# Optimization experiments

Hardware: AMD Instinct MI355X
Metric: run time of the kernel (lower is better)

The kernel has to match this reference:

```python
import jax, jax.numpy as jnp
import numpy as np

B, S, D, H = 2, 2048, 1024, 16
HD = D // H
SCALE = HD ** -0.5


def _xavier(key, fan_out, fan_in):
    limit = (6.0 / (fan_in + fan_out)) ** 0.5
    return jax.random.uniform(key, (fan_out, fan_in), jnp.float32, -limit, limit)


def setup_inputs() -> dict:
    key = jax.random.key(0)
    ks = jax.random.split(key, 11)
    return {
        "q": jax.random.normal(ks[0], (B, S, D), jnp.float32),
        "k": jax.random.normal(ks[1], (B, S, D), jnp.float32),
        "v": jax.random.normal(ks[2], (B, S, D), jnp.float32),
        "Wq": _xavier(ks[3], D, D), "bq": jnp.zeros((D,), jnp.float32),
        "Wk": _xavier(ks[4], D, D), "bk": jnp.zeros((D,), jnp.float32),
        "Wv": _xavier(ks[5], D, D), "bv": jnp.zeros((D,), jnp.float32),
        "Wo": _xavier(ks[6], D, D), "bo": jnp.zeros((D,), jnp.float32),
    }


def reference(q, k, v, Wq, bq, Wk, bk, Wv, bv, Wo, bo):
    # projections: torch Linear is x @ W.T + b
    def split_heads(x):  # [B,S,D] -> [B,H,S,HD]
        return x.reshape(B, S, H, HD).transpose(0, 2, 1, 3)

    qh = split_heads(q @ Wq.T + bq)
    kh = split_heads(k @ Wk.T + bk)
    vh = split_heads(v @ Wv.T + bv)

    scores = jnp.einsum('bhqd,bhkd->bhqk', qh, kh) * SCALE  # [B,H,S,S]
    attn = jax.nn.softmax(scores, axis=-1)
    out = jnp.einsum('bhqk,bhkd->bhqd', attn, vh)  # [B,H,S,HD]
    out = out.transpose(0, 2, 1, 3).reshape(B, S, D)
    return out @ Wo.T + bo
```

## Files before the change

kernel.cpp:

```cpp
#include <hip/hip_runtime.h>
#include <hip/hip_bf16.h>

typedef __attribute__((ext_vector_type(8))) short bf16x8;
typedef __attribute__((ext_vector_type(4))) float f32x4;
typedef __attribute__((ext_vector_type(16))) float f32x16;
typedef unsigned short u16;

#define MFMA16(A,B,C) __builtin_amdgcn_mfma_f32_16x16x32_bf16(A,B,C,0,0,0)
#define MFMA32(A,B,C) __builtin_amdgcn_mfma_f32_32x32x16_bf16(A,B,C,0,0,0)

__device__ __forceinline__ u16 f2bf(float f) {
    union { float f; unsigned u; } x{f};
    unsigned r = x.u + 0x7FFFu + ((x.u >> 16) & 1u);
    return (u16)(r >> 16);
}

__device__ __forceinline__ unsigned cvtpk(float lo, float hi) {
    unsigned r;
    asm("v_cvt_pk_bf16_f32 %0, %1, %2" : "=v"(r) : "v"(lo), "v"(hi));
    return r;
}

__device__ __forceinline__ void gload16(const void* src, void* dst) {
    __builtin_amdgcn_global_load_lds((const __attribute__((address_space(1))) void*)src,
                                     (__attribute__((address_space(3))) void*)dst, 16, 0, 0);
}

__device__ __forceinline__ void xhalf(unsigned lo, unsigned hi2, int hf, unsigned& j0, unsigned& j2) {
#if __has_builtin(__builtin_amdgcn_permlane32_swap)
    auto r = __builtin_amdgcn_permlane32_swap(lo, hi2, false, false);
    j0 = r[0]; j2 = r[1];
#else
    unsigned olo = (unsigned)__shfl_xor((int)lo, 32);
    unsigned ohi = (unsigned)__shfl_xor((int)hi2, 32);
    j0 = hf ? ohi : lo;
    j2 = hf ? hi2 : olo;
#endif
}

__global__ __launch_bounds__(256)
void cvt_all(const float* __restrict__ q, const float* __restrict__ k, const float* __restrict__ v,
             const float* __restrict__ Wq, const float* __restrict__ Wk,
             const float* __restrict__ Wv, const float* __restrict__ Wo,
             u16* __restrict__ oq, u16* __restrict__ ok, u16* __restrict__ ov,
             u16* __restrict__ ow) {
    int blk = blockIdx.x;
    const float* s;
    u16* o;
    if (blk < 6144) {
        int which = blk >> 11, lb = blk & 2047;
        s = (which == 0 ? q : (which == 1 ? k : v)) + (size_t)lb * 2048;
        o = (which == 0 ? oq : (which == 1 ? ok : ov)) + (size_t)lb * 2048;
    } else {
        int wblk = blk - 6144;
        int which = wblk >> 9, lb = wblk & 511;
        s = (which == 0 ? Wq : (which == 1 ? Wk : (which == 2 ? Wv : Wo))) + (size_t)lb * 2048;
        o = ow + (size_t)which * 1048576 + (size_t)lb * 2048;
    }
    size_t base = (size_t)threadIdx.x * 8;
    float4 v0 = *(const float4*)(s + base);
    float4 v1 = *(const float4*)(s + base + 4);
    bf16x8 rv;
    rv[0] = (short)f2bf(v0.x); rv[1] = (short)f2bf(v0.y); rv[2] = (short)f2bf(v0.z); rv[3] = (short)f2bf(v0.w);
    rv[4] = (short)f2bf(v1.x); rv[5] = (short)f2bf(v1.y); rv[6] = (short)f2bf(v1.z); rv[7] = (short)f2bf(v1.w);
    *(bf16x8*)(o + base) = rv;
}

template<int MODE>
__device__ __forceinline__ void gemm_body(u16* gsm, const u16* __restrict__ A, const u16* __restrict__ W,
                                          const float* __restrict__ bias, void* __restrict__ Cout,
                                          float scale) {
    u16* Asl = gsm;
    u16* Wsl = gsm + 16384;
    const int t = threadIdx.x;
    const int lane = t & 63, w = t >> 6;
    const int g = lane >> 4, c = lane & 15;
    const int bm = blockIdx.y * 128, bn = blockIdx.x * 64;
    const int wr = (w >> 1) * 64, wc = (w & 1) * 32;

    f32x4 acc[4][2];
    #pragma unroll
    for (int i = 0; i < 4; ++i) {
        acc[i][0] = f32x4{0.f, 0.f, 0.f, 0.f};
        acc[i][1] = f32x4{0.f, 0.f, 0.f, 0.f};
    }

#define GS(buf, k0)                                                                         \
    {                                                                                       \
        _Pragma("unroll")                                                                   \
        for (int i = 0; i < 4; ++i) {                                                       \
            int off = i * 4096 + w * 1024 + lane * 16;                                      \
            int row = off >> 7, sl = (off >> 4) & 7;                                        \
            gload16(A + (size_t)(bm + row) * 1024 + (k0) + ((sl ^ (row & 7)) << 3),         \
                    Asl + (buf) * 8192 + i * 2048 + w * 512);                               \
        }                                                                                   \
        _Pragma("unroll")                                                                   \
        for (int i = 0; i < 2; ++i) {                                                       \
            int off = i * 4096 + w * 1024 + lane * 16;                                      \
            int row = off >> 7, sl = (off >> 4) & 7;                                        \
            gload16(W + (size_t)(bn + row) * 1024 + (k0) + ((sl ^ (row & 7)) << 3),         \
                    Wsl + (buf) * 4096 + i * 2048 + w * 512);                               \
        }                                                                                   \
    }

    GS(0, 0);
    __syncthreads();
    int cur = 0;

    for (int k0 = 0; k0 < 1024; k0 += 64) {
        if (k0 < 960) GS(cur ^ 1, k0 + 64);
        #pragma unroll
        for (int ks = 0; ks < 2; ++ks) {
            bf16x8 af[4], bfr[2];
            #pragma unroll
            for (int rf = 0; rf < 4; ++rf) {
                int row = wr + rf * 16 + c;
                int col = (ks * 64 + g * 16) ^ ((row & 7) << 4);
                af[rf] = *(const bf16x8*)((const char*)Asl + cur * 16384 + row * 128 + col);
            }
            #pragma unroll
            for (int cf = 0; cf < 2; ++cf) {
                int row = wc + cf * 16 + c;
                int col = (ks * 64 + g * 16) ^ ((row & 7) << 4);
                bfr[cf] = *(const bf16x8*)((const char*)Wsl + cur * 8192 + row * 128 + col);
            }
            __builtin_amdgcn_s_setprio(1);
            #pragma unroll
            for (int rf = 0; rf < 4; ++rf)
                #pragma unroll
                for (int cf = 0; cf < 2; ++cf)
                    acc[rf][cf] = MFMA16(af[rf], bfr[cf], acc[rf][cf]);
            __builtin_amdgcn_s_setprio(0);
        }
        __syncthreads();
        cur ^= 1;
    }
#undef GS

    if (MODE == 2) {
        u16* trp = gsm;
        #pragma unroll
        for (int rf = 0; rf < 4; ++rf)
            #pragma unroll
            for (int cf = 0; cf < 2; ++cf) {
                int d = wc + cf * 16 + c;
                float bv = bias[bn + d];
                unsigned p0 = cvtpk(acc[rf][cf][0] + bv, acc[rf][cf][1] + bv);
                unsigned p1 = cvtpk(acc[rf][cf][2] + bv, acc[rf][cf][3] + bv);
                *(uint2*)&trp[d * 136 + wr + rf * 16 + 4 * g] = make_uint2(p0, p1);
            }
        __syncthreads();
        const int hb = bn >> 6, bb = bm >> 11, sb = bm & 2047;
        u16* vt = (u16*)Cout;
        #pragma unroll
        for (int i = 0; i < 4; ++i) {
            int fl = t + 256 * i;
            int d = fl >> 4, ch = fl & 15;
            bf16x8 vv = *(const bf16x8*)&trp[d * 136 + ch * 8];
            *(bf16x8*)(vt + ((size_t)((bb * 16 + hb) * 64 + d)) * 2048 + sb + ch * 8) = vv;
        }
        return;
    }

    #pragma unroll
    for (int rf = 0; rf < 4; ++rf) {
        #pragma unroll
        for (int cf = 0; cf < 2; ++cf) {
            int nCol = bn + wc + cf * 16 + c;
            float bv = bias[nCol];
            #pragma unroll
            for (int r = 0; r < 4; ++r) {
                int row = bm + wr + rf * 16 + 4 * g + r;
                float val = (acc[rf][cf][r] + bv) * scale;
                if (MODE == 1) ((float*)Cout)[(size_t)row * 1024 + nCol] = val;
                else           ((u16*)Cout)[(size_t)row * 1024 + nCol] = f2bf(val);
            }
        }
    }
}

__global__ __launch_bounds__(256)
void gemm_qkv(const u16* __restrict__ Ab, const u16* __restrict__ Wb,
              const float* __restrict__ b0, const float* __restrict__ b1, const float* __restrict__ b2,
              u16* __restrict__ Qp, u16* __restrict__ Kp, u16* __restrict__ Vtb, float qscale) {
    __shared__ u16 gsm[24576];
    int z = blockIdx.z;
    if (z == 0)      gemm_body<0>(gsm, Ab,           Wb,           b0, Qp,  qscale);
    else if (z == 1) gemm_body<0>(gsm, Ab + 4194304, Wb + 1048576, b1, Kp,  1.f);
    else             gemm_body<2>(gsm, Ab + 8388608, Wb + 2097152, b2, Vtb, 1.f);
}

__global__ __launch_bounds__(256)
void gemm_o(const u16* __restrict__ A, const u16* __restrict__ W,
            const float* __restrict__ bias, float* __restrict__ out) {
    __shared__ u16 gsm[24576];
    gemm_body<1>(gsm, A, W, bias, out, 1.f);
}

__global__ __launch_bounds__(512, 4)
void attn_mfma(const u16* __restrict__ Qp, const u16* __restrict__ Kp,
               const u16* __restrict__ Vt, u16* __restrict__ AO) {
    __shared__ u16 smem[40960];

    const int t = threadIdx.x, lane = t & 63, w = t >> 6;
    const int wl = w & 3, half = w >> 2;
    const int c5 = lane & 31, hf = lane >> 5;

    const int id = blockIdx.x;
    const int xcd = id & 7, slot = id >> 3;
    const int hd = xcd * 4 + (slot >> 4);
    const int b = hd >> 4, h = hd & 15;
    const int qw = (slot & 15) * 128 + wl * 32;

    bf16x8 qfr[4];
    #pragma unroll
    for (int ks = 0; ks < 4; ++ks)
        qfr[ks] = *(const bf16x8*)(Qp + (size_t)(b * 2048 + qw + c5) * 1024 + h * 64 + ks * 16 + hf * 8);

    f32x16 oacc[2], lacc;
    #pragma unroll
    for (int j = 0; j < 16; ++j) { oacc[0][j] = 0.f; oacc[1][j] = 0.f; lacc[j] = 0.f; }

    bf16x8 ones;
    #pragma unroll
    for (int j = 0; j < 8; ++j) ones[j] = (short)0x3F80;

#define STAGE(kbuf, vbuf, it)                                                                       \
    {                                                                                               \
        int row = t >> 3, sl = t & 7;                                                               \
        _Pragma("unroll")                                                                           \
        for (int i = 0; i < 2; ++i) {                                                               \
            int kti = i * 16 + (it);                                                                \
            const u16* srck = Kp + (size_t)(b * 2048 + kti * 64 + row) * 1024 + h * 64 +            \
                              ((sl ^ (row & 7)) << 3);                                              \
            gload16(srck, smem + i * 8192 + (kbuf) * 4096 + w * 512);                               \
            const u16* srcv = Vt + ((size_t)((b * 16 + h) * 64 + row)) * 2048 + kti * 64 +          \
                              ((sl ^ (row & 7)) << 3);                                              \
            gload16(srcv, smem + 16384 + i * 12288 + (vbuf) * 4096 + w * 512);                      \
        }                                                                                           \
    }

#define QKT(kbase, kf, s)                                                                           \
    {                                                                                               \
        _Pragma("unroll")                                                                           \
        for (int j = 0; j < 16; ++j) (s)[j] = 0.f;                                                  \
        const int krow = (kf) * 32 + c5;                                                            \
        const int ksw = (krow & 7) << 4;                                                            \
        _Pragma("unroll")                                                                           \
        for (int ks = 0; ks < 4; ++ks) {                                                            \
            bf16x8 ka = *(const bf16x8*)((kbase) + krow * 128 + ((ks * 32 + hf * 16) ^ ksw));       \
            (s) = MFMA32(ka, qfr[ks], (s));                                                         \
        }                                                                                           \
    }

#define SM(s, pv0, pv1)                                                                             \
    {                                                                                               \
        _Pragma("unroll")                                                                           \
        for (int j = 0; j < 16; ++j) (s)[j] = exp2f((s)[j]);                                        \
        unsigned wd[8];                                                                             \
        _Pragma("unroll")                                                                           \
        for (int j = 0; j < 8; ++j) wd[j] = cvtpk((s)[2 * j], (s)[2 * j + 1]);                      \
        union { unsigned u[4]; bf16x8 v; } a0, a1;                                                  \
        xhalf(wd[0], wd[2], hf, a0.u[0], a0.u[2]);                                                  \
        xhalf(wd[1], wd[3], hf, a0.u[1], a0.u[3]);                                                  \
        xhalf(wd[4], wd[6], hf, a1.u[0], a1.u[2]);                                                  \
        xhalf(wd[5], wd[7], hf, a1.u[1], a1.u[3]);                                                  \
        (pv0) = a0.v; (pv1) = a1.v;                                                                 \
    }

#define PVOP(vbase, kf, pv0, pv1)                                                                   \
    {                                                                                               \
        _Pragma("unroll")                                                                           \
        for (int pp = 0; pp < 2; ++pp) {                                                            \
            bf16x8 pB = pp ? (pv1) : (pv0);                                                         \
            const int kc = (kf) * 64 + pp * 32 + hf * 16;                                           \
            _Pragma("unroll")                                                                       \
            for (int df = 0; df < 2; ++df) {                                                        \
                int vrow = df * 32 + c5;                                                            \
                bf16x8 va = *(const bf16x8*)((vbase) + vrow * 128 + (kc ^ ((vrow & 7) << 4)));      \
                oacc[df] = MFMA32(va, pB, oacc[df]);                                                \
            }                                                                                       \
            lacc = MFMA32(ones, pB, lacc);                                                          \
        }                                                                                           \
    }

    STAGE(0, 0, 0);
    __syncthreads();

    const char* smb = (const char*)smem;
    const char* vreg = smb + 32768 + half * 24576;
    int cur2 = 0, cur3 = 0, nxt3 = 1, prv3 = 2;
    bf16x8 pc0, pc1;

    for (int it = 0; it < 16; ++it) {
        if (it < 15) STAGE(cur2 ^ 1, nxt3, it + 1);
        const char* kbase = smb + half * 16384 + cur2 * 8192;
        const char* vcur = vreg + cur3 * 8192;
        const char* vprev = vreg + prv3 * 8192;

        f32x16 s0;
        __builtin_amdgcn_s_setprio(1);
        QKT(kbase, 0, s0);
        if (it) PVOP(vprev, 1, pc0, pc1);
        __builtin_amdgcn_s_setprio(0);

        bf16x8 b00, b01;
        SM(s0, b00, b01);

        f32x16 s1;
        __builtin_amdgcn_s_setprio(1);
        QKT(kbase, 1, s1);
        PVOP(vcur, 0, b00, b01);
        __builtin_amdgcn_s_setprio(0);

        SM(s1, pc0, pc1);

        __syncthreads();
        prv3 = cur3; cur3 = nxt3; nxt3 = (nxt3 == 2) ? 0 : nxt3 + 1;
        cur2 ^= 1;
    }
    {
        const char* vprev = vreg + prv3 * 8192;
        PVOP(vprev, 1, pc0, pc1);
    }

    __syncthreads();
    float* fs = (float*)smem;
    const int pbase = wl * 2112;
    if (half) {
        #pragma unroll
        for (int df = 0; df < 2; ++df)
            #pragma unroll
            for (int j = 0; j < 16; ++j)
                fs[pbase + (df * 16 + j) * 64 + lane] = oacc[df][j];
        fs[pbase + 2048 + lane] = lacc[0];
    }
    __syncthreads();
    if (!half) {
        #pragma unroll
        for (int df = 0; df < 2; ++df)
            #pragma unroll
            for (int j = 0; j < 16; ++j)
                oacc[df][j] += fs[pbase + (df * 16 + j) * 64 + lane];
        const float inv = 1.f / (lacc[0] + fs[pbase + 2048 + lane]);

        char* pw = (char*)smem + 33792 + wl * 4096;
        #pragma unroll
        for (int df = 0; df < 2; ++df)
            #pragma unroll
            for (int rq = 0; rq < 4; ++rq) {
                unsigned p0 = cvtpk(oacc[df][rq * 4 + 0] * inv, oacc[df][rq * 4 + 1] * inv);
                unsigned p1 = cvtpk(oacc[df][rq * 4 + 2] * inv, oacc[df][rq * 4 + 3] * inv);
                int dbyte = df * 64 + rq * 16 + hf * 8;
                *(uint2*)(pw + c5 * 128 + (dbyte ^ ((c5 & 7) << 4))) = make_uint2(p0, p1);
            }
        #pragma unroll
        for (int i = 0; i < 4; ++i) {
            int fl = lane + 64 * i;
            int q = fl >> 3, ch = fl & 7;
            bf16x8 vv = *(const bf16x8*)(pw + q * 128 + ((ch * 16) ^ ((q & 7) << 4)));
            *(bf16x8*)(AO + (size_t)(b * 2048 + qw + q) * 1024 + h * 64 + ch * 8) = vv;
        }
    }
}

extern "C" void kernel_launch(void* const* d_in, const int* in_sizes, int n_in,
                              void* d_out, int out_size, void* d_ws, size_t ws_size,
                              hipStream_t stream) {
    const float* q  = (const float*)d_in[0];
    const float* k  = (const float*)d_in[1];
    const float* v  = (const float*)d_in[2];
    const float* Wq = (const float*)d_in[3];
    const float* bq = (const float*)d_in[4];
    const float* Wk = (const float*)d_in[5];
    const float* bk = (const float*)d_in[6];
    const float* Wv = (const float*)d_in[7];
    const float* bv = (const float*)d_in[8];
    const float* Wo = (const float*)d_in[9];
    const float* bo = (const float*)d_in[10];

    const size_t NE = 4194304;
    u16* ws = (u16*)d_ws;
    u16* xq = ws;
    u16* xk = ws + NE;
    u16* xv = ws + 2 * NE;
    u16* Wb = ws + 3 * NE;
    u16* Qp = ws + 4 * NE;
    u16* Kp = ws + 5 * NE;
    u16* Vtb = ws + 6 * NE;
    u16* AO = xk;

    const float CS = 0.125f * 1.4426950408889634f;

    cvt_all<<<8192, 256, 0, stream>>>(q, k, v, Wq, Wk, Wv, Wo, xq, xk, xv, Wb);

    gemm_qkv<<<dim3(16, 32, 3), 256, 0, stream>>>(ws, Wb, bq, bk, bv, Qp, Kp, Vtb, CS);

    attn_mfma<<<512, 512, 0, stream>>>(Qp, Kp, Vtb, AO);

    gemm_o<<<dim3(16, 32), 256, 0, stream>>>(AO, Wb + 3145728, bo, (float*)d_out);
}
```

Baseline: 120.9 us.

## Split attention KV halves into separate blocks with combine kernel; XCD-aware GEMM tiling

The attention kernel drops the in-block split across two 4-wave halves. Each KV half now runs as an independent 256-thread block, doubling the grid to 1024 blocks with half the LDS. Each block writes bf16-normalized partial outputs and row sums to workspace, and a new combine kernel merges them weighted by the row sums and writes AO. The GEMM launches are flattened to 1D grids with XCD-aware tile mapping for L2 locality. The price is an extra kernel launch, extra global traffic for the partials, and an added bf16 rounding step on the partial outputs.

```diff
diff --git a/kernel.cpp b/kernel.cpp
--- a/kernel.cpp
+++ b/kernel.cpp
@@ -13,6 +13,12 @@
     union { float f; unsigned u; } x{f};
     unsigned r = x.u + 0x7FFFu + ((x.u >> 16) & 1u);
     return (u16)(r >> 16);
+}
+
+__device__ __forceinline__ float bf2f(u16 x) {
+    union { unsigned u; float f; } y;
+    y.u = ((unsigned)x) << 16;
+    return y.f;
 }
 
 __device__ __forceinline__ unsigned cvtpk(float lo, float hi) {
@@ -69,13 +75,12 @@
 template<int MODE>
 __device__ __forceinline__ void gemm_body(u16* gsm, const u16* __restrict__ A, const u16* __restrict__ W,
                                           const float* __restrict__ bias, void* __restrict__ Cout,
-                                          float scale) {
+                                          float scale, int bm, int bn) {
     u16* Asl = gsm;
     u16* Wsl = gsm + 16384;
     const int t = threadIdx.x;
     const int lane = t & 63, w = t >> 6;
     const int g = lane >> 4, c = lane & 15;
-    const int bm = blockIdx.y * 128, bn = blockIdx.x * 64;
     const int wr = (w >> 1) * 64, wc = (w & 1) * 32;
 
     f32x4 acc[4][2];
@@ -184,33 +189,43 @@
               const float* __restrict__ b0, const float* __restrict__ b1, const float* __restrict__ b2,
               u16* __restrict__ Qp, u16* __restrict__ Kp, u16* __restrict__ Vtb, float qscale) {
     __shared__ u16 gsm[24576];
-    int z = blockIdx.z;
-    if (z == 0)      gemm_body<0>(gsm, Ab,           Wb,           b0, Qp,  qscale);
-    else if (z == 1) gemm_body<0>(gsm, Ab + 4194304, Wb + 1048576, b1, Kp,  1.f);
-    else             gemm_body<2>(gsm, Ab + 8388608, Wb + 2097152, b2, Vtb, 1.f);
+    int id = blockIdx.x;
+    int xcd = id & 7, r = id >> 3;
+    int z = r >> 6, rr = r & 63;
+    int bm = (xcd * 4 + (rr >> 4)) * 128;
+    int bn = (rr & 15) * 64;
+    if (z == 0)      gemm_body<0>(gsm, Ab,           Wb,           b0, Qp,  qscale, bm, bn);
+    else if (z == 1) gemm_body<0>(gsm, Ab + 4194304, Wb + 1048576, b1, Kp,  1.f, bm, bn);
+    else             gemm_body<2>(gsm, Ab + 8388608, Wb + 2097152, b2, Vtb, 1.f, bm, bn);
 }
 
 __global__ __launch_bounds__(256)
 void gemm_o(const u16* __restrict__ A, const u16* __restrict__ W,
             const float* __restrict__ bias, float* __restrict__ out) {
     __shared__ u16 gsm[24576];
-    gemm_body<1>(gsm, A, W, bias, out, 1.f);
-}
-
-__global__ __launch_bounds__(512, 4)
+    int id = blockIdx.x;
+    int xcd = id & 7, r = id >> 3;
+    int bm = (xcd * 4 + (r >> 4)) * 128;
+    int bn = (r & 15) * 64;
+    gemm_body<1>(gsm, A, W, bias, out, 1.f, bm, bn);
+}
+
+__global__ __launch_bounds__(256, 4)
 void attn_mfma(const u16* __restrict__ Qp, const u16* __restrict__ Kp,
-               const u16* __restrict__ Vt, u16* __restrict__ AO) {
-    __shared__ u16 smem[40960];
+               const u16* __restrict__ Vt, u16* __restrict__ op0, u16* __restrict__ op1,
+               float* __restrict__ lpart) {
+    __shared__ u16 smem[20480];
 
     const int t = threadIdx.x, lane = t & 63, w = t >> 6;
-    const int wl = w & 3, half = w >> 2;
     const int c5 = lane & 31, hf = lane >> 5;
 
     const int id = blockIdx.x;
-    const int xcd = id & 7, slot = id >> 3;
-    const int hd = xcd * 4 + (slot >> 4);
+    const int xcd = id & 7, r = id >> 3;
+    const int hd = xcd * 4 + (r >> 5);
+    const int rem = r & 31;
+    const int qblk = rem >> 1, half = rem & 1;
     const int b = hd >> 4, h = hd & 15;
-    const int qw = (slot & 15) * 128 + wl * 32;
+    const int qw = qblk * 128 + w * 32;
 
     bf16x8 qfr[4];
     #pragma unroll
@@ -227,16 +242,17 @@
 
 #define STAGE(kbuf, vbuf, it)                                                                       \
     {                                                                                               \
-        int row = t >> 3, sl = t & 7;                                                               \
-        _Pragma("unroll")                                                                           \
-        for (int i = 0; i < 2; ++i) {                                                               \
-            int kti = i * 16 + (it);                                                                \
+        const int kti = half * 16 + (it);                                                           \
+        _Pragma("unroll")                                                                           \
+        for (int i2 = 0; i2 < 2; ++i2) {                                                            \
+            int cch = t + 256 * i2;                                                                 \
+            int row = cch >> 3, sl = cch & 7;                                                       \
             const u16* srck = Kp + (size_t)(b * 2048 + kti * 64 + row) * 1024 + h * 64 +            \
                               ((sl ^ (row & 7)) << 3);                                              \
-            gload16(srck, smem + i * 8192 + (kbuf) * 4096 + w * 512);                               \
+            gload16(srck, smem + (kbuf) * 4096 + i2 * 2048 + w * 512);                              \
             const u16* srcv = Vt + ((size_t)((b * 16 + h) * 64 + row)) * 2048 + kti * 64 +          \
                               ((sl ^ (row & 7)) << 3);                                              \
-            gload16(srcv, smem + 16384 + i * 12288 + (vbuf) * 4096 + w * 512);                      \
+            gload16(srcv, smem + 8192 + (vbuf) * 4096 + i2 * 2048 + w * 512);                       \
         }                                                                                           \
     }
 
@@ -288,13 +304,13 @@
     __syncthreads();
 
     const char* smb = (const char*)smem;
-    const char* vreg = smb + 32768 + half * 24576;
+    const char* vreg = smb + 16384;
     int cur2 = 0, cur3 = 0, nxt3 = 1, prv3 = 2;
     bf16x8 pc0, pc1;
 
     for (int it = 0; it < 16; ++it) {
         if (it < 15) STAGE(cur2 ^ 1, nxt3, it + 1);
-        const char* kbase = smb + half * 16384 + cur2 * 8192;
+        const char* kbase = smb + cur2 * 8192;
         const char* vcur = vreg + cur3 * 8192;
         const char* vprev = vreg + prv3 * 8192;
 
@@ -324,43 +340,69 @@
         PVOP(vprev, 1, pc0, pc1);
     }
 
-    __syncthreads();
-    float* fs = (float*)smem;
-    const int pbase = wl * 2112;
-    if (half) {
-        #pragma unroll
-        for (int df = 0; df < 2; ++df)
-            #pragma unroll
-            for (int j = 0; j < 16; ++j)
-                fs[pbase + (df * 16 + j) * 64 + lane] = oacc[df][j];
-        fs[pbase + 2048 + lane] = lacc[0];
-    }
-    __syncthreads();
-    if (!half) {
-        #pragma unroll
-        for (int df = 0; df < 2; ++df)
-            #pragma unroll
-            for (int j = 0; j < 16; ++j)
-                oacc[df][j] += fs[pbase + (df * 16 + j) * 64 + lane];
-        const float inv = 1.f / (lacc[0] + fs[pbase + 2048 + lane]);
-
-        char* pw = (char*)smem + 33792 + wl * 4096;
-        #pragma unroll
-        for (int df = 0; df < 2; ++df)
-            #pragma unroll
-            for (int rq = 0; rq < 4; ++rq) {
-                unsigned p0 = cvtpk(oacc[df][rq * 4 + 0] * inv, oacc[df][rq * 4 + 1] * inv);
-                unsigned p1 = cvtpk(oacc[df][rq * 4 + 2] * inv, oacc[df][rq * 4 + 3] * inv);
-                int dbyte = df * 64 + rq * 16 + hf * 8;
-                *(uint2*)(pw + c5 * 128 + (dbyte ^ ((c5 & 7) << 4))) = make_uint2(p0, p1);
-            }
-        #pragma unroll
-        for (int i = 0; i < 4; ++i) {
-            int fl = lane + 64 * i;
-            int q = fl >> 3, ch = fl & 7;
-            bf16x8 vv = *(const bf16x8*)(pw + q * 128 + ((ch * 16) ^ ((q & 7) << 4)));
-            *(bf16x8*)(AO + (size_t)(b * 2048 + qw + q) * 1024 + h * 64 + ch * 8) = vv;
-        }
+    const int pbase = hd * 16 + qblk;
+    const float lh = lacc[0];
+    const float invh = 1.f / lh;
+    lpart[(pbase * 2 + half) * 256 + w * 64 + lane] = lh;
+
+    u16* op = (half ? op1 : op0) + (size_t)(pbase * 4 + w) * 2048 + lane * 32;
+    #pragma unroll
+    for (int df = 0; df < 2; ++df)
+        #pragma unroll
+        for (int rq = 0; rq < 4; ++rq) {
+            unsigned p0 = cvtpk(oacc[df][rq * 4 + 0] * invh, oacc[df][rq * 4 + 1] * invh);
+            unsigned p1 = cvtpk(oacc[df][rq * 4 + 2] * invh, oacc[df][rq * 4 + 3] * invh);
+            *(uint2*)&op[df * 16 + rq * 4] = make_uint2(p0, p1);
+        }
+}
+
+__global__ __launch_bounds__(256)
+void attn_combine(const u16* __restrict__ op0, const u16* __restrict__ op1,
+                  const float* __restrict__ lpart, u16* __restrict__ AO) {
+    __shared__ char pws[16384];
+    const int t = threadIdx.x, lane = t & 63, w = t >> 6;
+    const int c5 = lane & 31, hf = lane >> 5;
+    const int id = blockIdx.x;
+    const int hd = id >> 4, qblk = id & 15;
+    const int b = hd >> 4, h = hd & 15;
+    const int qw = qblk * 128 + w * 32;
+    const int pbase = hd * 16 + qblk;
+
+    const float l0 = lpart[(pbase * 2 + 0) * 256 + w * 64 + lane];
+    const float l1 = lpart[(pbase * 2 + 1) * 256 + w * 64 + lane];
+    const float inv = 1.f / (l0 + l1);
+    const float w0 = l0 * inv, w1 = l1 * inv;
+
+    const u16* o0 = op0 + (size_t)(pbase * 4 + w) * 2048 + lane * 32;
+    const u16* o1 = op1 + (size_t)(pbase * 4 + w) * 2048 + lane * 32;
+
+    char* pw = pws + w * 4096;
+    #pragma unroll
+    for (int df = 0; df < 2; ++df) {
+        bf16x8 a0 = *(const bf16x8*)(o0 + df * 16);
+        bf16x8 a1 = *(const bf16x8*)(o1 + df * 16);
+        bf16x8 c0 = *(const bf16x8*)(o0 + df * 16 + 8);
+        bf16x8 c1 = *(const bf16x8*)(o1 + df * 16 + 8);
+        float vals[16];
+        #pragma unroll
+        for (int j = 0; j < 8; ++j) {
+            vals[j]     = w0 * bf2f((u16)a0[j]) + w1 * bf2f((u16)a1[j]);
+            vals[8 + j] = w0 * bf2f((u16)c0[j]) + w1 * bf2f((u16)c1[j]);
+        }
+        #pragma unroll
+        for (int rq = 0; rq < 4; ++rq) {
+            unsigned p0 = cvtpk(vals[rq * 4 + 0], vals[rq * 4 + 1]);
+            unsigned p1 = cvtpk(vals[rq * 4 + 2], vals[rq * 4 + 3]);
+            int dbyte = df * 64 + rq * 16 + hf * 8;
+            *(uint2*)(pw + c5 * 128 + (dbyte ^ ((c5 & 7) << 4))) = make_uint2(p0, p1);
+        }
+    }
+    #pragma unroll
+    for (int i = 0; i < 4; ++i) {
+        int fl = lane + 64 * i;
+        int q = fl >> 3, ch = fl & 7;
+        bf16x8 vv = *(const bf16x8*)(pw + q * 128 + ((ch * 16) ^ ((q & 7) << 4)));
+        *(bf16x8*)(AO + (size_t)(b * 2048 + qw + q) * 1024 + h * 64 + ch * 8) = vv;
     }
 }
 
@@ -388,15 +430,18 @@
     u16* Qp = ws + 4 * NE;
     u16* Kp = ws + 5 * NE;
     u16* Vtb = ws + 6 * NE;
+    float* lpart = (float*)(ws + 7 * NE);
     u16* AO = xk;
 
     const float CS = 0.125f * 1.4426950408889634f;
 
     cvt_all<<<8192, 256, 0, stream>>>(q, k, v, Wq, Wk, Wv, Wo, xq, xk, xv, Wb);
 
-    gemm_qkv<<<dim3(16, 32, 3), 256, 0, stream>>>(ws, Wb, bq, bk, bv, Qp, Kp, Vtb, CS);
-
-    attn_mfma<<<512, 512, 0, stream>>>(Qp, Kp, Vtb, AO);
-
-    gemm_o<<<dim3(16, 32), 256, 0, stream>>>(AO, Wb + 3145728, bo, (float*)d_out);
-}
+    gemm_qkv<<<1536, 256, 0, stream>>>(ws, Wb, bq, bk, bv, Qp, Kp, Vtb, CS);
+
+    attn_mfma<<<1024, 256, 0, stream>>>(Qp, Kp, Vtb, xq, xv, lpart);
+
+    attn_combine<<<512, 256, 0, stream>>>(xq, xv, lpart, AO);
+
+    gemm_o<<<512, 256, 0, stream>>>(AO, Wb + 3145728, bo, (float*)d_out);
+}
```

Result: no change. 123.1 us (+1.8%).
